# Optimization experiments

Hardware: AMD Instinct MI355X
Metric: run time of the kernel (lower is better)

## Reference

```python
import jax, jax.numpy as jnp
import numpy as np

N_NODES = 50000
N_EDGES = 600000
D_IN = 128
D_HID = 1024
D_OUT = 128


def setup_inputs() -> dict:
    key = jax.random.key(0)
    ks = jax.random.split(key, 8)
    feat = jax.random.normal(ks[0], (N_NODES, D_IN), dtype=jnp.float32)
    edge_feat = jax.random.normal(ks[1], (N_EDGES, D_IN), dtype=jnp.float32)
    src = jax.random.randint(ks[2], (N_EDGES,), 0, N_NODES, dtype=jnp.int32)
    dst = jax.random.randint(ks[3], (N_EDGES,), 0, N_NODES, dtype=jnp.int32)
    W1 = jax.random.normal(ks[4], (D_IN, D_HID), dtype=jnp.float32) * (1.0 / np.sqrt(D_IN))
    b1 = jnp.zeros((D_HID,), dtype=jnp.float32)
    W2 = jax.random.normal(ks[5], (D_HID, D_OUT), dtype=jnp.float32) * (1.0 / np.sqrt(D_HID))
    b2 = jnp.zeros((D_OUT,), dtype=jnp.float32)
    return {"feat": feat, "edge_feat": edge_feat, "src": src, "dst": dst,
            "W1": W1, "b1": b1, "W2": W2, "b2": b2}


def reference(feat, edge_feat, src, dst, W1, b1, W2, b2):
    # DGL u_add_e: message m_e = h_src(e) + e_feat(e)   [E, D_IN]
    messages = feat[src] + edge_feat
    # reduce sum over incoming edges at each destination node -> [N, D_IN]
    h = jax.ops.segment_sum(messages, dst, num_segments=N_NODES)
    # 2-layer MLP
    h = jax.nn.relu(h @ W1 + b1)
    return h @ W2 + b2
```

## Files before the change

kernel.cpp:

```cpp
#include <hip/hip_runtime.h>
#include <hip/hip_bf16.h>

#define N_NODES 50000
#define N_EDGES 600000
#define D_IN    128
#define D_HID   1024
#define D_OUT   128

#define WS_H      0
#define WS_PAIRS  12800000
#define WS_OFF    17600000
#define WS_CURSOR 17800016
#define WS_DEG    18000016
#define WS_BSUM   18200016
#define WS_W1T    18201040
#define WS_W2T    18463184

typedef short bf16x8 __attribute__((ext_vector_type(8)));
typedef short s16x4  __attribute__((ext_vector_type(4)));
typedef float f32x4  __attribute__((ext_vector_type(4)));
typedef int   i32x2  __attribute__((ext_vector_type(2)));

__global__ __launch_bounds__(256) void hist_kernel(
    const int* __restrict__ dst, int* __restrict__ deg)
{
    int e = blockIdx.x * blockDim.x + threadIdx.x;
    if (e < N_EDGES) atomicAdd(&deg[dst[e]], 1);
}

__global__ __launch_bounds__(256) void scan1_kernel(
    const int* __restrict__ deg, int* __restrict__ bsum)
{
    __shared__ int red[256];
    int t = threadIdx.x;
    int idx = blockIdx.x * 256 + t;
    red[t] = (idx < N_NODES) ? deg[idx] : 0;
    __syncthreads();
    for (int s = 128; s > 0; s >>= 1) {
        if (t < s) red[t] += red[t + s];
        __syncthreads();
    }
    if (t == 0) bsum[blockIdx.x] = red[0];
}

#define SCAN_NB 196
__global__ __launch_bounds__(256) void scan2_kernel(
    int* __restrict__ bsum, int* __restrict__ off)
{
    __shared__ int sh[256];
    int t = threadIdx.x;
    int v = (t < SCAN_NB) ? bsum[t] : 0;
    sh[t] = v;
    __syncthreads();
    for (int ofs = 1; ofs < 256; ofs <<= 1) {
        int u = (t >= ofs) ? sh[t - ofs] : 0;
        __syncthreads();
        sh[t] += u;
        __syncthreads();
    }
    if (t < SCAN_NB) bsum[t] = sh[t] - v;
    if (t == 255) off[N_NODES] = sh[255];
}

__global__ __launch_bounds__(256) void scan3_kernel(
    const int* __restrict__ deg, const int* __restrict__ bsum,
    int* __restrict__ off, int* __restrict__ cursor)
{
    __shared__ int sh[256];
    int t = threadIdx.x;
    int idx = blockIdx.x * 256 + t;
    int v = (idx < N_NODES) ? deg[idx] : 0;
    sh[t] = v;
    __syncthreads();
    for (int ofs = 1; ofs < 256; ofs <<= 1) {
        int u = (t >= ofs) ? sh[t - ofs] : 0;
        __syncthreads();
        sh[t] += u;
        __syncthreads();
    }
    if (idx < N_NODES) {
        int ex = bsum[blockIdx.x] + sh[t] - v;
        off[idx] = ex;
        cursor[idx] = ex;
    }
}

__global__ __launch_bounds__(256) void fill_kernel(
    const int* __restrict__ dst, const int* __restrict__ src,
    int* __restrict__ cursor, int* __restrict__ pairs)
{
    int e = blockIdx.x * blockDim.x + threadIdx.x;
    if (e < N_EDGES) {
        int s = src[e];
        int pos = atomicAdd(&cursor[dst[e]], 1);
        i32x2 v; v.x = e; v.y = s;
        *(i32x2*)(pairs + 2 * (size_t)pos) = v;
    }
}

__global__ __launch_bounds__(256) void transpose_cvt2_kernel(
    const float* __restrict__ W1, __hip_bfloat16* __restrict__ w1t,
    const float* __restrict__ W2, __hip_bfloat16* __restrict__ w2t)
{
    __shared__ float tile[32][33];
    int b = blockIdx.x;
    const float* in;
    __hip_bfloat16* outp;
    int rows, cols, c0, r0;
    if (b < 128) {
        in = W1; outp = w1t; rows = D_IN; cols = D_HID;
        c0 = (b & 31) * 32; r0 = (b >> 5) * 32;
    } else {
        int bb = b - 128;
        in = W2; outp = w2t; rows = D_HID; cols = D_OUT;
        c0 = (bb & 3) * 32; r0 = (bb >> 2) * 32;
    }
    int tx = threadIdx.x & 31, ty = threadIdx.x >> 5;
    #pragma unroll
    for (int i = 0; i < 32; i += 8)
        tile[ty + i][tx] = in[(size_t)(r0 + ty + i) * cols + (c0 + tx)];
    __syncthreads();
    #pragma unroll
    for (int i = 0; i < 32; i += 8)
        outp[(size_t)(c0 + ty + i) * rows + (r0 + tx)] =
            __float2bfloat16(tile[tx][ty + i]);
}

__global__ __launch_bounds__(256) void gather_kernel(
    const float* __restrict__ feat,
    const float* __restrict__ edge_feat,
    const int*   __restrict__ pairs,
    const int*   __restrict__ off,
    __hip_bfloat16* __restrict__ hbf)
{
    const int wv   = threadIdx.x >> 6;
    const int lane = threadIdx.x & 63;
    const int n = blockIdx.x * 4 + wv;
    if (n >= N_NODES) return;

    int i   = __builtin_amdgcn_readfirstlane(off[n]);
    int end = __builtin_amdgcn_readfirstlane(off[n + 1]);

    float2 a0 = make_float2(0.f, 0.f), a1 = a0, a2 = a0, a3 = a0;

    for (; i + 8 <= end; i += 8) {
        i32x2 p0 = *(const i32x2*)(pairs + 2 * (size_t)(i + 0));
        i32x2 p1 = *(const i32x2*)(pairs + 2 * (size_t)(i + 1));
        i32x2 p2 = *(const i32x2*)(pairs + 2 * (size_t)(i + 2));
        i32x2 p3 = *(const i32x2*)(pairs + 2 * (size_t)(i + 3));
        i32x2 p4 = *(const i32x2*)(pairs + 2 * (size_t)(i + 4));
        i32x2 p5 = *(const i32x2*)(pairs + 2 * (size_t)(i + 5));
        i32x2 p6 = *(const i32x2*)(pairs + 2 * (size_t)(i + 6));
        i32x2 p7 = *(const i32x2*)(pairs + 2 * (size_t)(i + 7));
        float2 e0 = ((const float2*)(edge_feat + (size_t)p0.x * D_IN))[lane];
        float2 g0 = ((const float2*)(feat      + (size_t)p0.y * D_IN))[lane];
        float2 e1 = ((const float2*)(edge_feat + (size_t)p1.x * D_IN))[lane];
        float2 g1 = ((const float2*)(feat      + (size_t)p1.y * D_IN))[lane];
        float2 e2 = ((const float2*)(edge_feat + (size_t)p2.x * D_IN))[lane];
        float2 g2 = ((const float2*)(feat      + (size_t)p2.y * D_IN))[lane];
        float2 e3 = ((const float2*)(edge_feat + (size_t)p3.x * D_IN))[lane];
        float2 g3 = ((const float2*)(feat      + (size_t)p3.y * D_IN))[lane];
        float2 e4 = ((const float2*)(edge_feat + (size_t)p4.x * D_IN))[lane];
        float2 g4 = ((const float2*)(feat      + (size_t)p4.y * D_IN))[lane];
        float2 e5 = ((const float2*)(edge_feat + (size_t)p5.x * D_IN))[lane];
        float2 g5 = ((const float2*)(feat      + (size_t)p5.y * D_IN))[lane];
        float2 e6 = ((const float2*)(edge_feat + (size_t)p6.x * D_IN))[lane];
        float2 g6 = ((const float2*)(feat      + (size_t)p6.y * D_IN))[lane];
        float2 e7 = ((const float2*)(edge_feat + (size_t)p7.x * D_IN))[lane];
        float2 g7 = ((const float2*)(feat      + (size_t)p7.y * D_IN))[lane];
        a0.x += e0.x + g0.x;  a0.y += e0.y + g0.y;
        a1.x += e1.x + g1.x;  a1.y += e1.y + g1.y;
        a2.x += e2.x + g2.x;  a2.y += e2.y + g2.y;
        a3.x += e3.x + g3.x;  a3.y += e3.y + g3.y;
        a0.x += e4.x + g4.x;  a0.y += e4.y + g4.y;
        a1.x += e5.x + g5.x;  a1.y += e5.y + g5.y;
        a2.x += e6.x + g6.x;  a2.y += e6.y + g6.y;
        a3.x += e7.x + g7.x;  a3.y += e7.y + g7.y;
    }
    for (; i + 2 <= end; i += 2) {
        i32x2 p0 = *(const i32x2*)(pairs + 2 * (size_t)(i + 0));
        i32x2 p1 = *(const i32x2*)(pairs + 2 * (size_t)(i + 1));
        float2 e0 = ((const float2*)(edge_feat + (size_t)p0.x * D_IN))[lane];
        float2 g0 = ((const float2*)(feat      + (size_t)p0.y * D_IN))[lane];
        float2 e1 = ((const float2*)(edge_feat + (size_t)p1.x * D_IN))[lane];
        float2 g1 = ((const float2*)(feat      + (size_t)p1.y * D_IN))[lane];
        a0.x += e0.x + g0.x;  a0.y += e0.y + g0.y;
        a1.x += e1.x + g1.x;  a1.y += e1.y + g1.y;
    }
    if (i < end) {
        i32x2 p = *(const i32x2*)(pairs + 2 * (size_t)i);
        float2 e = ((const float2*)(edge_feat + (size_t)p.x * D_IN))[lane];
        float2 g = ((const float2*)(feat      + (size_t)p.y * D_IN))[lane];
        a0.x += e.x + g.x;  a0.y += e.y + g.y;
    }
    float sx = (a0.x + a1.x) + (a2.x + a3.x);
    float sy = (a0.y + a1.y) + (a2.y + a3.y);
    __hip_bfloat162 hv;
    hv.x = __float2bfloat16(sx);
    hv.y = __float2bfloat16(sy);
    ((__hip_bfloat162*)(hbf + (size_t)n * D_IN))[lane] = hv;
}

#define QS_STRIDE 136

__global__ __launch_bounds__(256) void mlp_mfma_kernel(
    const __hip_bfloat16* __restrict__ hbf,
    const __hip_bfloat16* __restrict__ w1t,
    const float* __restrict__ b1,
    const __hip_bfloat16* __restrict__ w2t,
    const float* __restrict__ b2,
    float* __restrict__ out)
{
    __shared__ __align__(16) short q_s[2][64 * QS_STRIDE];

    const int t    = threadIdx.x;
    const int wv   = t >> 6;
    const int lane = t & 63;
    const int half = lane >> 4;
    const int lid  = lane & 15;
    const int nb   = blockIdx.x * 64;

    const short* hs  = (const short*)hbf;
    const short* w1s = (const short*)w1t;
    const short* w2s = (const short*)w2t;

    bf16x8 hfrag[4][4];
    #pragma unroll
    for (int nt = 0; nt < 4; ++nt) {
        int row = nb + nt * 16 + lid;
        if (row >= N_NODES) row = N_NODES - 1;
        #pragma unroll
        for (int ks = 0; ks < 4; ++ks)
            hfrag[nt][ks] = *(const bf16x8*)&hs[(size_t)row * 128 + ks * 32 + half * 8];
    }

    f32x4 acc[4][2];
    #pragma unroll
    for (int mt = 0; mt < 4; ++mt) {
        acc[mt][0] = f32x4{0.f, 0.f, 0.f, 0.f};
        acc[mt][1] = f32x4{0.f, 0.f, 0.f, 0.f};
    }

    int pb = 0;
    for (int jb = 0; jb < D_HID; jb += 128, pb ^= 1) {
        #pragma unroll
        for (int ht = 0; ht < 2; ++ht) {
            const int hid0 = jb + wv * 32 + ht * 16;
            bf16x8 w1f[4];
            #pragma unroll
            for (int ks = 0; ks < 4; ++ks)
                w1f[ks] = *(const bf16x8*)&w1s[(size_t)(hid0 + lid) * 128 + ks * 32 + half * 8];
            f32x4 bias4 = *(const f32x4*)&b1[hid0 + half * 4];
            #pragma unroll
            for (int nt = 0; nt < 4; ++nt) {
                f32x4 c = bias4;
                #pragma unroll
                for (int ks = 0; ks < 4; ++ks)
                    c = __builtin_amdgcn_mfma_f32_16x16x32_bf16(w1f[ks], hfrag[nt][ks], c, 0, 0, 0);
                s16x4 hv;
                #pragma unroll
                for (int r = 0; r < 4; ++r) {
                    float v = fmaxf(c[r], 0.f);
                    __hip_bfloat16 bv = __float2bfloat16(v);
                    hv[r] = *(short*)&bv;
                }
                *(s16x4*)&q_s[pb][(nt * 16 + lid) * QS_STRIDE + wv * 32 + ht * 16 + half * 4] = hv;
            }
        }
        __syncthreads();

        #pragma unroll
        for (int kh = 0; kh < 2; ++kh) {
            bf16x8 a2f[4][2];
            #pragma unroll
            for (int mt = 0; mt < 4; ++mt)
                #pragma unroll
                for (int ks = 0; ks < 2; ++ks)
                    a2f[mt][ks] = *(const bf16x8*)&q_s[pb][(mt * 16 + lid) * QS_STRIDE + kh * 64 + ks * 32 + half * 8];
            #pragma unroll
            for (int nt = 0; nt < 2; ++nt) {
                #pragma unroll
                for (int ks = 0; ks < 2; ++ks) {
                    bf16x8 b2f = *(const bf16x8*)&w2s[(size_t)(wv * 32 + nt * 16 + lid) * 1024 + jb + kh * 64 + ks * 32 + half * 8];
                    #pragma unroll
                    for (int mt = 0; mt < 4; ++mt)
                        acc[mt][nt] = __builtin_amdgcn_mfma_f32_16x16x32_bf16(a2f[mt][ks], b2f, acc[mt][nt], 0, 0, 0);
                }
            }
        }
    }

    #pragma unroll
    for (int nt = 0; nt < 2; ++nt) {
        int col = wv * 32 + nt * 16 + lid;
        float bv = b2[col];
        #pragma unroll
        for (int mt = 0; mt < 4; ++mt) {
            #pragma unroll
            for (int r = 0; r < 4; ++r) {
                int row = nb + mt * 16 + half * 4 + r;
                if (row < N_NODES)
                    out[(size_t)row * D_OUT + col] = acc[mt][nt][r] + bv;
            }
        }
    }
}

extern "C" void kernel_launch(void* const* d_in, const int* in_sizes, int n_in,
                              void* d_out, int out_size, void* d_ws, size_t ws_size,
                              hipStream_t stream) {
    const float* feat      = (const float*)d_in[0];
    const float* edge_feat = (const float*)d_in[1];
    const int*   src       = (const int*)d_in[2];
    const int*   dst       = (const int*)d_in[3];
    const float* W1        = (const float*)d_in[4];
    const float* b1        = (const float*)d_in[5];
    const float* W2        = (const float*)d_in[6];
    const float* b2        = (const float*)d_in[7];
    float* out = (float*)d_out;

    char* ws = (char*)d_ws;
    __hip_bfloat16* hbf = (__hip_bfloat16*)(ws + WS_H);
    int*   pairs  = (int*)(ws + WS_PAIRS);
    int*   off    = (int*)(ws + WS_OFF);
    int*   cursor = (int*)(ws + WS_CURSOR);
    int*   deg    = (int*)(ws + WS_DEG);
    int*   bsum   = (int*)(ws + WS_BSUM);
    __hip_bfloat16* w1t = (__hip_bfloat16*)(ws + WS_W1T);
    __hip_bfloat16* w2t = (__hip_bfloat16*)(ws + WS_W2T);

    hipMemsetAsync(deg, 0, (size_t)N_NODES * sizeof(int), stream);

    hist_kernel<<<(N_EDGES + 255) / 256, 256, 0, stream>>>(dst, deg);
    scan1_kernel<<<SCAN_NB, 256, 0, stream>>>(deg, bsum);
    scan2_kernel<<<1, 256, 0, stream>>>(bsum, off);
    scan3_kernel<<<SCAN_NB, 256, 0, stream>>>(deg, bsum, off, cursor);
    fill_kernel<<<(N_EDGES + 255) / 256, 256, 0, stream>>>(dst, src, cursor, pairs);

    transpose_cvt2_kernel<<<256, 256, 0, stream>>>(W1, w1t, W2, w2t);

    gather_kernel<<<(N_NODES + 3) / 4, 256, 0, stream>>>(
        feat, edge_feat, pairs, off, hbf);

    mlp_mfma_kernel<<<(N_NODES + 63) / 64, 256, 0, stream>>>(
        hbf, w1t, b1, w2t, b2, out);
}
```

Before: 605.3 us.

## Fuse CSR build and weight transpose into one cooperative kernel with grid syncs

Replaces the memset, histogram, three scan kernels, the fill kernel and the weight transpose/convert with a single cooperative kernel of 196 blocks that uses grid-wide syncs between phases. The aim is to remove several kernel launches and inter-kernel gaps in the CSR construction. The trade-off is that only 196 blocks do the edge-wide atomic histogram and fill, so those phases get less parallelism, and each grid sync has a cost of its own.

```diff
diff --git a/kernel.cpp b/kernel.cpp
--- a/kernel.cpp
+++ b/kernel.cpp
@@ -1,5 +1,8 @@
 #include <hip/hip_runtime.h>
 #include <hip/hip_bf16.h>
+#include <hip/hip_cooperative_groups.h>
+
+namespace cg = cooperative_groups;
 
 #define N_NODES 50000
 #define N_EDGES 600000
@@ -21,109 +24,107 @@
 typedef float f32x4  __attribute__((ext_vector_type(4)));
 typedef int   i32x2  __attribute__((ext_vector_type(2)));
 
-__global__ __launch_bounds__(256) void hist_kernel(
-    const int* __restrict__ dst, int* __restrict__ deg)
+#define CSR_NB 196
+
+__global__ __launch_bounds__(256) void csr_build_kernel(
+    const int* __restrict__ dst, const int* __restrict__ src,
+    int* __restrict__ deg, int* __restrict__ bsum,
+    int* __restrict__ off, int* __restrict__ cursor,
+    int* __restrict__ pairs,
+    const float* __restrict__ W1, __hip_bfloat16* __restrict__ w1t,
+    const float* __restrict__ W2, __hip_bfloat16* __restrict__ w2t)
 {
-    int e = blockIdx.x * blockDim.x + threadIdx.x;
-    if (e < N_EDGES) atomicAdd(&deg[dst[e]], 1);
-}
-
-__global__ __launch_bounds__(256) void scan1_kernel(
-    const int* __restrict__ deg, int* __restrict__ bsum)
-{
-    __shared__ int red[256];
-    int t = threadIdx.x;
-    int idx = blockIdx.x * 256 + t;
-    red[t] = (idx < N_NODES) ? deg[idx] : 0;
-    __syncthreads();
-    for (int s = 128; s > 0; s >>= 1) {
-        if (t < s) red[t] += red[t + s];
-        __syncthreads();
-    }
-    if (t == 0) bsum[blockIdx.x] = red[0];
-}
-
-#define SCAN_NB 196
-__global__ __launch_bounds__(256) void scan2_kernel(
-    int* __restrict__ bsum, int* __restrict__ off)
-{
-    __shared__ int sh[256];
-    int t = threadIdx.x;
-    int v = (t < SCAN_NB) ? bsum[t] : 0;
-    sh[t] = v;
-    __syncthreads();
-    for (int ofs = 1; ofs < 256; ofs <<= 1) {
-        int u = (t >= ofs) ? sh[t - ofs] : 0;
-        __syncthreads();
-        sh[t] += u;
-        __syncthreads();
-    }
-    if (t < SCAN_NB) bsum[t] = sh[t] - v;
-    if (t == 255) off[N_NODES] = sh[255];
-}
-
-__global__ __launch_bounds__(256) void scan3_kernel(
-    const int* __restrict__ deg, const int* __restrict__ bsum,
-    int* __restrict__ off, int* __restrict__ cursor)
-{
-    __shared__ int sh[256];
-    int t = threadIdx.x;
-    int idx = blockIdx.x * 256 + t;
-    int v = (idx < N_NODES) ? deg[idx] : 0;
-    sh[t] = v;
-    __syncthreads();
-    for (int ofs = 1; ofs < 256; ofs <<= 1) {
-        int u = (t >= ofs) ? sh[t - ofs] : 0;
-        __syncthreads();
-        sh[t] += u;
-        __syncthreads();
-    }
-    if (idx < N_NODES) {
-        int ex = bsum[blockIdx.x] + sh[t] - v;
-        off[idx] = ex;
-        cursor[idx] = ex;
-    }
-}
-
-__global__ __launch_bounds__(256) void fill_kernel(
-    const int* __restrict__ dst, const int* __restrict__ src,
-    int* __restrict__ cursor, int* __restrict__ pairs)
-{
-    int e = blockIdx.x * blockDim.x + threadIdx.x;
-    if (e < N_EDGES) {
+    cg::grid_group grid = cg::this_grid();
+    __shared__ int   sh[256];
+    __shared__ float tile[32][33];
+
+    const int t   = threadIdx.x;
+    const int b   = blockIdx.x;
+    const int gid = b * 256 + t;
+    const int gsz = CSR_NB * 256;
+
+    for (int i = gid; i < N_NODES; i += gsz) deg[i] = 0;
+    grid.sync();
+
+    for (int e = gid; e < N_EDGES; e += gsz) atomicAdd(&deg[dst[e]], 1);
+    grid.sync();
+
+    {
+        int idx = gid;
+        sh[t] = (idx < N_NODES) ? deg[idx] : 0;
+        __syncthreads();
+        for (int s = 128; s > 0; s >>= 1) {
+            if (t < s) sh[t] += sh[t + s];
+            __syncthreads();
+        }
+        if (t == 0) bsum[b] = sh[0];
+    }
+    grid.sync();
+
+    if (b == 0) {
+        int v = (t < CSR_NB) ? bsum[t] : 0;
+        sh[t] = v;
+        __syncthreads();
+        for (int ofs = 1; ofs < 256; ofs <<= 1) {
+            int u = (t >= ofs) ? sh[t - ofs] : 0;
+            __syncthreads();
+            sh[t] += u;
+            __syncthreads();
+        }
+        if (t < CSR_NB) bsum[t] = sh[t] - v;
+        if (t == 255) off[N_NODES] = sh[255];
+    }
+    grid.sync();
+
+    {
+        int idx = gid;
+        int v = (idx < N_NODES) ? deg[idx] : 0;
+        sh[t] = v;
+        __syncthreads();
+        for (int ofs = 1; ofs < 256; ofs <<= 1) {
+            int u = (t >= ofs) ? sh[t - ofs] : 0;
+            __syncthreads();
+            sh[t] += u;
+            __syncthreads();
+        }
+        if (idx < N_NODES) {
+            int ex = bsum[b] + sh[t] - v;
+            off[idx] = ex;
+            cursor[idx] = ex;
+        }
+    }
+    grid.sync();
+
+    for (int e = gid; e < N_EDGES; e += gsz) {
         int s = src[e];
         int pos = atomicAdd(&cursor[dst[e]], 1);
         i32x2 v; v.x = e; v.y = s;
         *(i32x2*)(pairs + 2 * (size_t)pos) = v;
     }
-}
-
-__global__ __launch_bounds__(256) void transpose_cvt2_kernel(
-    const float* __restrict__ W1, __hip_bfloat16* __restrict__ w1t,
-    const float* __restrict__ W2, __hip_bfloat16* __restrict__ w2t)
-{
-    __shared__ float tile[32][33];
-    int b = blockIdx.x;
-    const float* in;
-    __hip_bfloat16* outp;
-    int rows, cols, c0, r0;
-    if (b < 128) {
-        in = W1; outp = w1t; rows = D_IN; cols = D_HID;
-        c0 = (b & 31) * 32; r0 = (b >> 5) * 32;
-    } else {
-        int bb = b - 128;
-        in = W2; outp = w2t; rows = D_HID; cols = D_OUT;
-        c0 = (bb & 3) * 32; r0 = (bb >> 2) * 32;
-    }
-    int tx = threadIdx.x & 31, ty = threadIdx.x >> 5;
-    #pragma unroll
-    for (int i = 0; i < 32; i += 8)
-        tile[ty + i][tx] = in[(size_t)(r0 + ty + i) * cols + (c0 + tx)];
-    __syncthreads();
-    #pragma unroll
-    for (int i = 0; i < 32; i += 8)
-        outp[(size_t)(c0 + ty + i) * rows + (r0 + tx)] =
-            __float2bfloat16(tile[tx][ty + i]);
+
+    for (int tt = b; tt < 256; tt += CSR_NB) {
+        const float* in;
+        __hip_bfloat16* outp;
+        int rows, cols, c0, r0;
+        if (tt < 128) {
+            in = W1; outp = w1t; rows = D_IN; cols = D_HID;
+            c0 = (tt & 31) * 32; r0 = (tt >> 5) * 32;
+        } else {
+            int bb = tt - 128;
+            in = W2; outp = w2t; rows = D_HID; cols = D_OUT;
+            c0 = (bb & 3) * 32; r0 = (bb >> 2) * 32;
+        }
+        int tx = t & 31, ty = t >> 5;
+        __syncthreads();
+        #pragma unroll
+        for (int i = 0; i < 32; i += 8)
+            tile[ty + i][tx] = in[(size_t)(r0 + ty + i) * cols + (c0 + tx)];
+        __syncthreads();
+        #pragma unroll
+        for (int i = 0; i < 32; i += 8)
+            outp[(size_t)(c0 + ty + i) * rows + (r0 + tx)] =
+                __float2bfloat16(tile[tx][ty + i]);
+    }
 }
 
 __global__ __launch_bounds__(256) void gather_kernel(
@@ -329,15 +330,15 @@
     __hip_bfloat16* w1t = (__hip_bfloat16*)(ws + WS_W1T);
     __hip_bfloat16* w2t = (__hip_bfloat16*)(ws + WS_W2T);
 
-    hipMemsetAsync(deg, 0, (size_t)N_NODES * sizeof(int), stream);
-
-    hist_kernel<<<(N_EDGES + 255) / 256, 256, 0, stream>>>(dst, deg);
-    scan1_kernel<<<SCAN_NB, 256, 0, stream>>>(deg, bsum);
-    scan2_kernel<<<1, 256, 0, stream>>>(bsum, off);
-    scan3_kernel<<<SCAN_NB, 256, 0, stream>>>(deg, bsum, off, cursor);
-    fill_kernel<<<(N_EDGES + 255) / 256, 256, 0, stream>>>(dst, src, cursor, pairs);
-
-    transpose_cvt2_kernel<<<256, 256, 0, stream>>>(W1, w1t, W2, w2t);
+    {
+        void* args[] = {
+            (void*)&dst, (void*)&src, (void*)&deg, (void*)&bsum,
+            (void*)&off, (void*)&cursor, (void*)&pairs,
+            (void*)&W1, (void*)&w1t, (void*)&W2, (void*)&w2t
+        };
+        hipLaunchCooperativeKernel((const void*)csr_build_kernel,
+                                   dim3(CSR_NB), dim3(256), args, 0, stream);
+    }
 
     gather_kernel<<<(N_NODES + 3) / 4, 256, 0, stream>>>(
         feat, edge_feat, pairs, off, hbf);
```

After: 715.5 us. 18.2% more time.
